# Kernel optimization log

Hardware: AMD Instinct MI355X
Metric: run time of the kernel (lower is better)

The kernel has to match this reference:

```python
import jax, jax.numpy as jnp
import numpy as np

H = 64  # hidden size

def setup_inputs() -> dict:
    key = jax.random.key(0)
    ks = jax.random.split(key, 7)
    B, T = 256, 5000
    s = 1.0 / np.sqrt(H)  # PyTorch LSTM init scale
    return {
        "x":    jax.random.normal(ks[0], (B, T), dtype=jnp.float32),
        "W_ih": jax.random.uniform(ks[1], (4 * H, 1), jnp.float32, -s, s),
        "W_hh": jax.random.uniform(ks[2], (4 * H, H), jnp.float32, -s, s),
        "b_ih": jax.random.uniform(ks[3], (4 * H,), jnp.float32, -s, s),
        "b_hh": jax.random.uniform(ks[4], (4 * H,), jnp.float32, -s, s),
        "W_fc": jax.random.uniform(ks[5], (128, H), jnp.float32, -s, s),
        "b_fc": jax.random.uniform(ks[6], (128,), jnp.float32, -s, s),
    }

def _lstm_last_hidden(x, W_ih, W_hh, b_ih, b_hh):
    # x: [B, T]; returns last hidden state h_T: [B, H]
    B, T = x.shape
    # input projection for all timesteps at once: [B, T, 4H]
    # (input_size == 1, so this is an outer product with W_ih[:, 0])
    x_proj = x[:, :, None] * W_ih[:, 0][None, None, :] + (b_ih + b_hh)

    def step(carry, xp_t):
        h, c = carry
        gates = xp_t + h @ W_hh.T  # [B, 4H]
        i = jax.nn.sigmoid(gates[:, 0 * H:1 * H])
        f = jax.nn.sigmoid(gates[:, 1 * H:2 * H])
        g = jnp.tanh(gates[:, 2 * H:3 * H])
        o = jax.nn.sigmoid(gates[:, 3 * H:4 * H])
        c = f * c + i * g
        h = o * jnp.tanh(c)
        return (h, c), None

    h0 = jnp.zeros((B, H), x.dtype)
    c0 = jnp.zeros((B, H), x.dtype)
    (h, c), _ = jax.lax.scan(step, (h0, c0), jnp.swapaxes(x_proj, 0, 1))
    return h

def reference(x, W_ih, W_hh, b_ih, b_hh, W_fc, b_fc):
    h_last = _lstm_last_hidden(x, W_ih, W_hh, b_ih, b_hh)  # [B, H]
    return jax.nn.relu(h_last @ W_fc.T + b_fc)  # [B, 128]
```

## Files before the change

kernel.cpp:

```cpp
#include <hip/hip_runtime.h>


#define LSTM_H 64
#define LSTM_T 5000
#define LSTM_B 256

__device__ __forceinline__ float fast_rcp(float v) {
    return __builtin_amdgcn_rcpf(v);
}

template<int J>
__device__ __forceinline__ float row_ror(float v) {
    return __builtin_bit_cast(float,
        __builtin_amdgcn_mov_dpp(__builtin_bit_cast(int, v),
                                 0x120 + J, 0xF, 0xF, false));
}

template<int K>
__device__ __forceinline__ float quad_bcast(float v) {
    constexpr int ctrl = K | (K << 2) | (K << 4) | (K << 6);
    return __builtin_bit_cast(float,
        __builtin_amdgcn_mov_dpp(__builtin_bit_cast(int, v),
                                 ctrl, 0xF, 0xF, false));
}

__global__ __launch_bounds__(256, 1) void ECGLSTM_lstm_dpp(
    const float* __restrict__ x,
    const float* __restrict__ W_ih,
    const float* __restrict__ W_hh,
    const float* __restrict__ b_ih,
    const float* __restrict__ b_hh,
    const float* __restrict__ W_fc,
    const float* __restrict__ b_fc,
    float* __restrict__ out)
{
    const int tid  = threadIdx.x;
    const int lane = tid & 63;
    const int w    = tid >> 6;
    const int g    = lane & 3;
    const int ul   = lane >> 2;
    const int u    = w * 16 + ul;
    const int b    = blockIdx.x;

    __shared__ float xch[LSTM_T];
    __shared__ float hbuf[2][LSTM_H];

    const float* xb = x + b * LSTM_T;
    for (int i = tid; i < LSTM_T; i += 256) xch[i] = xb[i];

    int dirp = __builtin_amdgcn_mov_dpp(lane, 0x121, 0xF, 0xF, false);
    const int e = (__builtin_amdgcn_readlane(dirp, 0) == 1) ? 1 : -1;

    const int row = g * LSTM_H + u;
    float wrot[LSTM_H];
    #pragma unroll
    for (int m = 0; m < LSTM_H; ++m) {
        const int cc = m >> 4, jj = m & 15;
        const int k  = (((lane & 48) | ((lane + e * jj) & 15)) ^ (cc << 4));
        wrot[m] = W_hh[row * LSTM_H + k];
    }

    const float wih  = W_ih[row];
    const float bias = b_ih[row] + b_hh[row];
    const bool  is_t = (g == 2);
    const float aexp = is_t ? -2.0f : -1.0f;
    const float smul = is_t ?  2.0f :  1.0f;
    const float dadd = is_t ? -1.0f :  0.0f;

    float c = 0.0f;
    if (tid < LSTM_H) hbuf[0][tid] = 0.0f;
    __syncthreads();

    #define RF(cN, j) a##cN = fmaf(row_ror<j>(b##cN), wrot[16 * cN + j], a##cN);
    #define CHUNK(cN)                                                          \
        float a##cN = b##cN * wrot[16 * cN];                                   \
        RF(cN, 1)  RF(cN, 2)  RF(cN, 3)  RF(cN, 4)  RF(cN, 5)                  \
        RF(cN, 6)  RF(cN, 7)  RF(cN, 8)  RF(cN, 9)  RF(cN, 10)                 \
        RF(cN, 11) RF(cN, 12) RF(cN, 13) RF(cN, 14) RF(cN, 15)

    #define LSTM_STEP(t, P)                                                    \
    {                                                                          \
        const float xv = xch[(t)];                          \
        const float* hb = hbuf[(P)];                                           \
        float b0 = hb[lane];                                \
        float b1 = hb[lane ^ 16];                                              \
        float b2 = hb[lane ^ 32];                                              \
        float b3 = hb[lane ^ 48];                                              \
        CHUNK(0) CHUNK(1) CHUNK(2) CHUNK(3)                                    \
        float dot = (a0 + a1) + (a2 + a3);                                     \
        float gv  = fmaf(xv, wih, bias) + dot;                                 \
        float ex  = __expf(aexp * gv);                                         \
        float act = fmaf(smul, fast_rcp(1.0f + ex), dadd);                     \
        float i_  = quad_bcast<0>(act);                                        \
        float f_  = quad_bcast<1>(act);                                        \
        float g_  = quad_bcast<2>(act);                                        \
        float o_  = quad_bcast<3>(act);                                        \
        c = fmaf(f_, c, i_ * g_);                                              \
        float e2 = __expf(2.0f * c);                                           \
        float th = 1.0f - 2.0f * fast_rcp(e2 + 1.0f);                          \
        if (g == 0) hbuf[1 - (P)][u] = o_ * th;             \
        __syncthreads();                                  \
    }

    for (int t = 0; t < LSTM_T; t += 2) {
        LSTM_STEP(t, 0);
        LSTM_STEP(t + 1, 1);
    }
    #undef LSTM_STEP
    #undef CHUNK
    #undef RF

    if (tid < 128) {
        float s = b_fc[tid];
        const float4* wf = reinterpret_cast<const float4*>(W_fc + tid * LSTM_H);
        const float4* h4 = reinterpret_cast<const float4*>(hbuf[0]);
        #pragma unroll
        for (int i = 0; i < LSTM_H / 4; ++i) {
            float4 wv = wf[i];
            float4 hv = h4[i];
            s = fmaf(hv.x, wv.x, s);
            s = fmaf(hv.y, wv.y, s);
            s = fmaf(hv.z, wv.z, s);
            s = fmaf(hv.w, wv.w, s);
        }
        out[b * 128 + tid] = fmaxf(s, 0.0f);
    }
}

extern "C" void kernel_launch(void* const* d_in, const int* in_sizes, int n_in,
                              void* d_out, int out_size, void* d_ws, size_t ws_size,
                              hipStream_t stream) {
    const float* x    = (const float*)d_in[0];
    const float* W_ih = (const float*)d_in[1];
    const float* W_hh = (const float*)d_in[2];
    const float* b_ih = (const float*)d_in[3];
    const float* b_hh = (const float*)d_in[4];
    const float* W_fc = (const float*)d_in[5];
    const float* b_fc = (const float*)d_in[6];
    float* out = (float*)d_out;

    ECGLSTM_lstm_dpp<<<LSTM_B, 256, 0, stream>>>(
        x, W_ih, W_hh, b_ih, b_hh, W_fc, b_fc, out);
}
```

Measured before the change: 2.394 ms.

## Split LSTM hidden-dot reduction across two half-waves with bpermute combine

Doubles threads per block to 512 so each gate row's 64-wide recurrent dot product is split into two 32-element halves held by lanes in opposite half-waves. Each thread reads h as float4 from LDS and rotates within DPP rows, then combines partial sums with ds_bpermute. Per-thread weight registers halve to 32 and the serial FMA chain shortens, at the cost of an extra cross-lane exchange and more waves taking part in each per-step barrier.

```diff
diff --git a/kernel.cpp b/kernel.cpp
--- a/kernel.cpp
+++ b/kernel.cpp
@@ -24,7 +24,7 @@
                                  ctrl, 0xF, 0xF, false));
 }
 
-__global__ __launch_bounds__(256, 1) void ECGLSTM_lstm_dpp(
+__global__ __launch_bounds__(512, 2) void ECGLSTM_lstm_ksplit(
     const float* __restrict__ x,
     const float* __restrict__ W_ih,
     const float* __restrict__ W_hh,
@@ -38,26 +38,31 @@
     const int lane = tid & 63;
     const int w    = tid >> 6;
     const int g    = lane & 3;
-    const int ul   = lane >> 2;
-    const int u    = w * 16 + ul;
+    const int ul   = (lane >> 2) & 7;
+    const int kh   = lane >> 5;
+    const int u    = w * 8 + ul;
     const int b    = blockIdx.x;
 
     __shared__ float xch[LSTM_T];
     __shared__ float hbuf[2][LSTM_H];
 
     const float* xb = x + b * LSTM_T;
-    for (int i = tid; i < LSTM_T; i += 256) xch[i] = xb[i];
+    for (int i = tid; i < LSTM_T; i += 512) xch[i] = xb[i];
 
-    int dirp = __builtin_amdgcn_mov_dpp(lane, 0x121, 0xF, 0xF, false);
+    int dirp = __builtin_amdgcn_mov_dpp(lane & 15, 0x121, 0xF, 0xF, false);
     const int e = (__builtin_amdgcn_readlane(dirp, 0) == 1) ? 1 : -1;
 
+    const int p  = lane & 15;
+    const int c0 = (p >> 1) + 8 * kh;
+
     const int row = g * LSTM_H + u;
-    float wrot[LSTM_H];
+    float wrotc[32];
     #pragma unroll
-    for (int m = 0; m < LSTM_H; ++m) {
-        const int cc = m >> 4, jj = m & 15;
-        const int k  = (((lane & 48) | ((lane + e * jj) & 15)) ^ (cc << 4));
-        wrot[m] = W_hh[row * LSTM_H + k];
+    for (int j = 0; j < 8; ++j) {
+        const int cj = ((((p >> 1) + e * j) & 7) + 8 * kh);
+        #pragma unroll
+        for (int i = 0; i < 4; ++i)
+            wrotc[4 * j + i] = W_hh[row * LSTM_H + 4 * cj + i];
     }
 
     const float wih  = W_ih[row];
@@ -67,28 +72,32 @@
     const float smul = is_t ?  2.0f :  1.0f;
     const float dadd = is_t ? -1.0f :  0.0f;
 
+    const int bperm_addr = (lane ^ 32) << 2;
+
     float c = 0.0f;
     if (tid < LSTM_H) hbuf[0][tid] = 0.0f;
     __syncthreads();
 
-    #define RF(cN, j) a##cN = fmaf(row_ror<j>(b##cN), wrot[16 * cN + j], a##cN);
-    #define CHUNK(cN)                                                          \
-        float a##cN = b##cN * wrot[16 * cN];                                   \
-        RF(cN, 1)  RF(cN, 2)  RF(cN, 3)  RF(cN, 4)  RF(cN, 5)                  \
-        RF(cN, 6)  RF(cN, 7)  RF(cN, 8)  RF(cN, 9)  RF(cN, 10)                 \
-        RF(cN, 11) RF(cN, 12) RF(cN, 13) RF(cN, 14) RF(cN, 15)
+    #define ROT4(j)                                                            \
+        a0 = fmaf(row_ror<2*(j)>(hv.x), wrotc[4*(j)],     a0);                 \
+        a1 = fmaf(row_ror<2*(j)>(hv.y), wrotc[4*(j) + 1], a1);                 \
+        a2 = fmaf(row_ror<2*(j)>(hv.z), wrotc[4*(j) + 2], a2);                 \
+        a3 = fmaf(row_ror<2*(j)>(hv.w), wrotc[4*(j) + 3], a3);
 
     #define LSTM_STEP(t, P)                                                    \
     {                                                                          \
+        const float4 hv = reinterpret_cast<const float4*>(hbuf[(P)])[c0];      \
         const float xv = xch[(t)];                          \
-        const float* hb = hbuf[(P)];                                           \
-        float b0 = hb[lane];                                \
-        float b1 = hb[lane ^ 16];                                              \
-        float b2 = hb[lane ^ 32];                                              \
-        float b3 = hb[lane ^ 48];                                              \
-        CHUNK(0) CHUNK(1) CHUNK(2) CHUNK(3)                                    \
-        float dot = (a0 + a1) + (a2 + a3);                                     \
-        float gv  = fmaf(xv, wih, bias) + dot;                                 \
+        float a0 = hv.x * wrotc[0];                                            \
+        float a1 = hv.y * wrotc[1];                                            \
+        float a2 = hv.z * wrotc[2];                                            \
+        float a3 = hv.w * wrotc[3];                                            \
+        ROT4(1) ROT4(2) ROT4(3) ROT4(4) ROT4(5) ROT4(6) ROT4(7)                \
+        float half_dot = (a0 + a1) + (a2 + a3);                                \
+        float other = __builtin_bit_cast(float,                                \
+            __builtin_amdgcn_ds_bpermute(bperm_addr,                           \
+                __builtin_bit_cast(int, half_dot)));                           \
+        float gv  = fmaf(xv, wih, bias) + (half_dot + other);                  \
         float ex  = __expf(aexp * gv);                                         \
         float act = fmaf(smul, fast_rcp(1.0f + ex), dadd);                     \
         float i_  = quad_bcast<0>(act);                                        \
@@ -98,7 +107,7 @@
         c = fmaf(f_, c, i_ * g_);                                              \
         float e2 = __expf(2.0f * c);                                           \
         float th = 1.0f - 2.0f * fast_rcp(e2 + 1.0f);                          \
-        if (g == 0) hbuf[1 - (P)][u] = o_ * th;             \
+        if ((lane & 35) == 0) hbuf[1 - (P)][u] = o_ * th;   \
         __syncthreads();                                  \
     }
 
@@ -107,8 +116,7 @@
         LSTM_STEP(t + 1, 1);
     }
     #undef LSTM_STEP
-    #undef CHUNK
-    #undef RF
+    #undef ROT4
 
     if (tid < 128) {
         float s = b_fc[tid];
@@ -139,6 +147,6 @@
     const float* b_fc = (const float*)d_in[6];
     float* out = (float*)d_out;
 
-    ECGLSTM_lstm_dpp<<<LSTM_B, 256, 0, stream>>>(
+    ECGLSTM_lstm_ksplit<<<LSTM_B, 512, 0, stream>>>(
         x, W_ih, W_hh, b_ih, b_hh, W_fc, b_fc, out);
 }
```

Result: faster. 2.326 ms (-2.8%).
